# Kernel optimization log

Hardware: AMD Instinct MI355X
Metric: run time of the kernel (lower is better)

Reference implementation:

```python
import jax, jax.numpy as jnp
import numpy as np

B, N, F_IN, T = 4, 10000, 16, 12
E = 160000
K = 3
C_CHEB = 64
C_TIME = 64
LN_EPS = 1e-5


def _lambda_max(row, col, n):
    # Power iteration on the unnormalized Laplacian L = D - A (what
    # LaplacianLambdaMax computes with normalization=None).
    deg = np.bincount(row, minlength=n).astype(np.float64)
    rng = np.random.default_rng(123)
    v = rng.standard_normal(n)
    v /= np.linalg.norm(v)
    for _ in range(100):
        agg = np.zeros(n)
        np.add.at(agg, col, v[row])
        w = deg * v - agg
        v = w / max(np.linalg.norm(w), 1e-12)
    agg = np.zeros(n)
    np.add.at(agg, col, v[row])
    return np.float32(v @ (deg * v - agg))


def setup_inputs() -> dict:
    rng = np.random.default_rng(0)
    ei = rng.integers(0, N, size=(2, E))
    lam = _lambda_max(ei[0], ei[1], N)
    key = jax.random.key(0)
    k = jax.random.split(key, 8)
    sF = 1.0 / np.sqrt(F_IN)
    sC = 1.0 / np.sqrt(3 * C_CHEB)
    return {
        "x": jax.random.normal(k[0], (B, N, F_IN, T), jnp.float32),
        "edge_index": jnp.asarray(ei, dtype=jnp.int32),
        "lambda_max": jnp.float32(lam),
        "cheb_W": jax.random.normal(k[1], (K, F_IN, C_CHEB), jnp.float32) * sF,
        "cheb_b": jax.random.normal(k[2], (C_CHEB,), jnp.float32) * 0.01,
        "time_W": jax.random.normal(k[3], (C_TIME, C_CHEB, 1, 3), jnp.float32) * sC,
        "time_b": jax.random.normal(k[4], (C_TIME,), jnp.float32) * 0.01,
        "res_W": jax.random.normal(k[5], (C_TIME, F_IN, 1, 1), jnp.float32) * sF,
        "res_b": jax.random.normal(k[6], (C_TIME,), jnp.float32) * 0.01,
        "ln_gamma": jnp.ones((C_TIME,), jnp.float32),
        "ln_beta": jnp.zeros((C_TIME,), jnp.float32),
    }


def reference(x, edge_index, lambda_max, cheb_W, cheb_b, time_W, time_b,
              res_W, res_b, ln_gamma, ln_beta):
    Bb, Nn, Fin, Tt = x.shape
    row, col = edge_index[0], edge_index[1]
    # deg from scatter of unit edge weights at row (PyG get_laplacian)
    deg = jax.ops.segment_sum(jnp.ones(row.shape[0], x.dtype), row, num_segments=Nn)

    # --- ChebConv over all (batch, time) slices jointly ---
    # (B,N,F,T) -> (N, B*T, F): node axis leading for gather/scatter
    v = jnp.transpose(x, (1, 0, 3, 2)).reshape(Nn, Bb * Tt, Fin)

    def Lhat(u):  # scaled Laplacian L_hat = 2(D - A)/lambda_max - I
        agg = jax.ops.segment_sum(u[row], col, num_segments=Nn)
        return (2.0 / lambda_max) * (deg[:, None, None] * u - agg) - u

    Tx0 = v
    out = jnp.einsum('nbf,fc->nbc', Tx0, cheb_W[0])
    Tx1 = Lhat(Tx0)
    out = out + jnp.einsum('nbf,fc->nbc', Tx1, cheb_W[1])
    for k in range(2, cheb_W.shape[0]):
        Tx2 = 2.0 * Lhat(Tx1) - Tx0
        out = out + jnp.einsum('nbf,fc->nbc', Tx2, cheb_W[k])
        Tx0, Tx1 = Tx1, Tx2
    spatial = jax.nn.relu(out + cheb_b)  # (N, B*T, C_cheb)

    # (N, B*T, C) -> (B, C, N, T) for NCHW temporal conv
    spatial = spatial.reshape(Nn, Bb, Tt, C_CHEB)
    spatial = jnp.transpose(spatial, (1, 3, 0, 2))  # (B,C,N,T)

    dn = ('NCHW', 'OIHW', 'NCHW')
    tc = jax.lax.conv_general_dilated(spatial, time_W, (1, 1), ((0, 0), (1, 1)),
                                      dimension_numbers=dn) + time_b[None, :, None, None]
    xr = jnp.transpose(x, (0, 2, 1, 3))  # (B,F,N,T)
    res = jax.lax.conv_general_dilated(xr, res_W, (1, 1), ((0, 0), (0, 0)),
                                       dimension_numbers=dn) + res_b[None, :, None, None]

    h = jax.nn.relu(res + tc)                  # (B, C_time, N, T)
    h = jnp.transpose(h, (0, 3, 2, 1))         # (B, T, N, C_time)
    mu = jnp.mean(h, axis=-1, keepdims=True)
    var = jnp.mean((h - mu) ** 2, axis=-1, keepdims=True)
    hn = (h - mu) * jax.lax.rsqrt(var + LN_EPS) * ln_gamma + ln_beta
    return jnp.transpose(hn, (0, 2, 3, 1))     # (B, N, C_time, T)
```

## Files before the change

### kernel.cpp

```cpp
#include <hip/hip_runtime.h>

typedef short bf16x8 __attribute__((ext_vector_type(8)));
typedef float f32x4 __attribute__((ext_vector_type(4)));

#define NN 10000
#define EE 160000
#define BB 4
#define TTT 12
#define FFF 16
#define CCC 64
#define BT 48
#define NF 768
#define SLOTS 64

#define TCS 72
#define SPS 72
#define HMS 68

#define WS_DEG     0u
#define WS_CNT     40960u
#define WS_CWT     81920u
#define WS_RWTB    90112u
#define WS_WKT     94208u
#define WS_CSRP    118784u
#define WS_VBF     2678784u
#define WS_TX1BF   18040320u

__device__ __forceinline__ unsigned short f2bf(float x){
    unsigned int u = __float_as_uint(x);
    u += 0x7FFFu + ((u >> 16) & 1u);
    return (unsigned short)(u >> 16);
}
__device__ __forceinline__ float bf2f(unsigned short h){
    return __uint_as_float(((unsigned int)h) << 16);
}

#define GMIN4(E)                                                                  \
    E.x = E.x < NN ? E.x : NN; E.y = E.y < NN ? E.y : NN;                         \
    E.z = E.z < NN ? E.z : NN; E.w = E.w < NN ? E.w : NN;

#define GATHER8(SRC, EA, EB, ACC0, ACC1, ACC2, ACC3, Q)                           \
    {                                                                             \
        ushort4 p0 = *(const ushort4*)&SRC[(size_t)EA.x * NF + (Q) * 4];          \
        ushort4 p1 = *(const ushort4*)&SRC[(size_t)EA.y * NF + (Q) * 4];          \
        ushort4 p2 = *(const ushort4*)&SRC[(size_t)EA.z * NF + (Q) * 4];          \
        ushort4 p3 = *(const ushort4*)&SRC[(size_t)EA.w * NF + (Q) * 4];          \
        ushort4 p4 = *(const ushort4*)&SRC[(size_t)EB.x * NF + (Q) * 4];          \
        ushort4 p5 = *(const ushort4*)&SRC[(size_t)EB.y * NF + (Q) * 4];          \
        ushort4 p6 = *(const ushort4*)&SRC[(size_t)EB.z * NF + (Q) * 4];          \
        ushort4 p7 = *(const ushort4*)&SRC[(size_t)EB.w * NF + (Q) * 4];          \
        ACC0 += bf2f(p0.x)+bf2f(p1.x)+bf2f(p2.x)+bf2f(p3.x)                       \
              + bf2f(p4.x)+bf2f(p5.x)+bf2f(p6.x)+bf2f(p7.x);                      \
        ACC1 += bf2f(p0.y)+bf2f(p1.y)+bf2f(p2.y)+bf2f(p3.y)                       \
              + bf2f(p4.y)+bf2f(p5.y)+bf2f(p6.y)+bf2f(p7.y);                      \
        ACC2 += bf2f(p0.z)+bf2f(p1.z)+bf2f(p2.z)+bf2f(p3.z)                       \
              + bf2f(p4.z)+bf2f(p5.z)+bf2f(p6.z)+bf2f(p7.z);                      \
        ACC3 += bf2f(p0.w)+bf2f(p1.w)+bf2f(p2.w)+bf2f(p3.w)                       \
              + bf2f(p4.w)+bf2f(p5.w)+bf2f(p6.w)+bf2f(p7.w);                      \
    }

__global__ __launch_bounds__(256) void k_setup(
    const float* __restrict__ x, const int* __restrict__ ei,
    const float* __restrict__ chW, const float* __restrict__ tW, const float* __restrict__ rW,
    float* __restrict__ deg, int* __restrict__ cnt, int* __restrict__ csrp,
    unsigned short* __restrict__ vbf, unsigned short* __restrict__ tx1bf,
    unsigned short* __restrict__ cWt, unsigned short* __restrict__ rWtb,
    unsigned short* __restrict__ wkt)
{
    int bid = blockIdx.x, tid = threadIdx.x;
    if (bid < 625){
        int e = bid * 256 + tid;
        if (e < EE) atomicAdd(&deg[ei[e]], 1.0f);
    } else if (bid < 1250){
        int e = (bid - 625) * 256 + tid;
        if (e < EE){
            int c = ei[EE + e];
            int slot = atomicAdd(&cnt[c], 1);
            if (slot < SLOTS) csrp[c * SLOTS + slot] = ei[e];
        }
    } else if (bid < 3125){
        int u = (bid - 1250) * 256 + tid;
        int n = u / 48, r = u - n * 48;
        int t = r >> 2, j = r & 3;
        #pragma unroll
        for (int b = 0; b < BB; ++b){
            const float* xp = x + (size_t)(b * NN + n) * 192;
            ushort4 w = { f2bf(xp[(4 * j + 0) * 12 + t]),
                          f2bf(xp[(4 * j + 1) * 12 + t]),
                          f2bf(xp[(4 * j + 2) * 12 + t]),
                          f2bf(xp[(4 * j + 3) * 12 + t]) };
            *(ushort4*)&vbf[(size_t)n * NF + b * 192 + t * 16 + j * 4] = w;
        }
    } else if (bid == 3125){
        if (tid < 192){
            ushort4 z = { 0, 0, 0, 0 };
            *(ushort4*)&vbf[(size_t)NN * NF + tid * 4]   = z;
            *(ushort4*)&tx1bf[(size_t)NN * NF + tid * 4] = z;
        }
    } else {
        int idx = (bid - 3126) * 256 + tid;
        if (idx < 4096){
            int c = idx >> 6, k = idx & 63;
            float v = 0.f;
            if (k < 48){ int kk = k >> 4, f = k & 15; v = chW[kk * 1024 + f * 64 + c]; }
            cWt[idx] = f2bf(v);
        } else if (idx < 6144){
            int j = idx - 4096;
            int o = j >> 5, k = j & 31;
            float v = (k < 16) ? rW[o * 16 + k] : 0.f;
            rWtb[j] = f2bf(v);
        } else {
            int j = idx - 6144;
            int kk = j >> 12; int r2 = j & 4095;
            int o = r2 >> 6, dc = r2 & 63;
            wkt[j] = f2bf(tW[(o * 64 + dc) * 3 + kk]);
        }
    }
}

__global__ __launch_bounds__(192) void k_lhat(
        const unsigned short* __restrict__ vbf, const float* __restrict__ deg,
        const int* __restrict__ cnt, const int* __restrict__ csrp,
        const float* __restrict__ lam, unsigned short* __restrict__ tx1bf){
    int n = blockIdx.x;
    int q = threadIdx.x;
    float s2 = 2.0f / lam[0];
    float dn = deg[n];
    int c = cnt[n]; c = c > SLOTS ? SLOTS : c;
    int iters = (c + 15) >> 4;
    const int4* cp = (const int4*)(csrp + n * SLOTS);
    float a0 = 0.f, a1 = 0.f, a2 = 0.f, a3 = 0.f;
    for (int it = 0; it < iters; ++it){
        int4 e0 = cp[it * 4], e1 = cp[it * 4 + 1];
        int4 e2 = cp[it * 4 + 2], e3 = cp[it * 4 + 3];
        GMIN4(e0) GMIN4(e1) GMIN4(e2) GMIN4(e3)
        GATHER8(vbf, e0, e1, a0, a1, a2, a3, q);
        GATHER8(vbf, e2, e3, a0, a1, a2, a3, q);
    }
    ushort4 hv = *(const ushort4*)&vbf[(size_t)n * NF + q * 4];
    float v0 = bf2f(hv.x), v1 = bf2f(hv.y), v2 = bf2f(hv.z), v3 = bf2f(hv.w);
    ushort4 o4 = { f2bf(s2 * (dn * v0 - a0) - v0),
                   f2bf(s2 * (dn * v1 - a1) - v1),
                   f2bf(s2 * (dn * v2 - a2) - v2),
                   f2bf(s2 * (dn * v3 - a3) - v3) };
    *(ushort4*)&tx1bf[(size_t)n * NF + q * 4] = o4;
}

__global__ __launch_bounds__(256) void k_fused(
    const unsigned short* __restrict__ vbf, const unsigned short* __restrict__ tx1bf,
    const float* __restrict__ deg, const int* __restrict__ cnt, const int* __restrict__ csrp,
    const float* __restrict__ lam,
    const unsigned short* __restrict__ cWt, const float* __restrict__ chebB,
    const unsigned short* __restrict__ wkt, const float* __restrict__ timeB,
    const unsigned short* __restrict__ rWtb, const float* __restrict__ resB,
    const float* __restrict__ gamma, const float* __restrict__ beta,
    float* __restrict__ out)
{
    __shared__ __align__(16) char smem[21120];
    unsigned short* spl  = (unsigned short*)smem;
    float2*         red  = (float2*)smem;
    unsigned short* tcat = (unsigned short*)(smem + 8064);
    float*          hmat = (float*)(smem + 8064);

    int n = blockIdx.x;
    int tid = threadIdx.x;

    {
        int rid = tid >> 5;
        int cc = tid & 31;
        int b = rid >> 1, p = (rid & 1) * 13;
        *(unsigned int*)&spl[(b * 14 + p) * SPS + cc * 2] = 0u;
    }

    if (tid < 192){
        float s2 = 2.0f / lam[0];
        float dn = deg[n];
        ushort4 hv = *(const ushort4*)&vbf[(size_t)n * NF + tid * 4];
        ushort4 hu = *(const ushort4*)&tx1bf[(size_t)n * NF + tid * 4];
        float a0 = 0.f, a1 = 0.f, a2 = 0.f, a3 = 0.f;
        int c = cnt[n]; c = c > SLOTS ? SLOTS : c;
        int iters = (c + 7) >> 3;
        const int4* cp = (const int4*)(csrp + n * SLOTS);
        for (int it = 0; it < iters; ++it){
            int4 e0 = cp[it * 2], e1 = cp[it * 2 + 1];
            GMIN4(e0) GMIN4(e1)
            GATHER8(tx1bf, e0, e1, a0, a1, a2, a3, tid);
        }
        float u0 = bf2f(hu.x), u1 = bf2f(hu.y), u2 = bf2f(hu.z), u3 = bf2f(hu.w);
        float v0 = bf2f(hv.x), v1 = bf2f(hv.y), v2 = bf2f(hv.z), v3 = bf2f(hv.w);
        ushort4 w2 = { f2bf(2.0f * (s2 * (dn * u0 - a0) - u0) - v0),
                       f2bf(2.0f * (s2 * (dn * u1 - a1) - u1) - v1),
                       f2bf(2.0f * (s2 * (dn * u2 - a2) - u2) - v2),
                       f2bf(2.0f * (s2 * (dn * u3 - a3) - u3) - v3) };
        ushort4 zz = { 0, 0, 0, 0 };
        int bt = tid >> 2, ch = tid & 3;
        *(ushort4*)&tcat[bt * TCS +      ch * 4] = hv;
        *(ushort4*)&tcat[bt * TCS + 16 + ch * 4] = hu;
        *(ushort4*)&tcat[bt * TCS + 32 + ch * 4] = w2;
        *(ushort4*)&tcat[bt * TCS + 48 + ch * 4] = zz;
    }
    __syncthreads();

    int lane = tid & 63;
    int nt   = tid >> 6;
    int ln   = lane & 15;
    int quad = lane >> 4;
    int q8   = quad * 8;
    int col  = nt * 16 + ln;

    {
        bf16x8 cb0 = *(const bf16x8*)&cWt[col * 64 + q8];
        bf16x8 cb1 = *(const bf16x8*)&cWt[col * 64 + 32 + q8];
        bf16x8 rb  = *(const bf16x8*)&rWtb[col * 32 + q8];
        f32x4 cacc[3], racc[3];
        #pragma unroll
        for (int mt = 0; mt < 3; ++mt){
            bf16x8 a0 = *(const bf16x8*)&tcat[(mt * 16 + ln) * TCS + q8];
            bf16x8 a1 = *(const bf16x8*)&tcat[(mt * 16 + ln) * TCS + 32 + q8];
            f32x4 z = {0.f, 0.f, 0.f, 0.f};
            cacc[mt] = __builtin_amdgcn_mfma_f32_16x16x32_bf16(a0, cb0, z, 0, 0, 0);
            cacc[mt] = __builtin_amdgcn_mfma_f32_16x16x32_bf16(a1, cb1, cacc[mt], 0, 0, 0);
            racc[mt] = __builtin_amdgcn_mfma_f32_16x16x32_bf16(a0, rb, z, 0, 0, 0);
        }
        float cb = chebB[col];
        #pragma unroll
        for (int mt = 0; mt < 3; ++mt){
            #pragma unroll
            for (int i = 0; i < 4; ++i){
                int r = mt * 16 + quad * 4 + i;
                int bb = (r * 43) >> 9;
                int tt = r - 12 * bb;
                float val = fmaxf(cacc[mt][i] + cb, 0.0f);
                spl[(bb * 14 + tt + 1) * SPS + col] = f2bf(val);
            }
        }
        __syncthreads();

        bf16x8 wb[3][2];
        #pragma unroll
        for (int kk = 0; kk < 3; ++kk){
            wb[kk][0] = *(const bf16x8*)&wkt[kk * 4096 + col * 64 + q8];
            wb[kk][1] = *(const bf16x8*)&wkt[kk * 4096 + col * 64 + 32 + q8];
        }
        float tb = timeB[col] + resB[col];
        #pragma unroll
        for (int mt = 0; mt < 3; ++mt){
            int bt = mt * 16 + ln;
            int bb = (bt * 43) >> 9;
            int tt = bt - 12 * bb;
            int rbase = bb * 14 + tt;
            f32x4 tacc = {0.f, 0.f, 0.f, 0.f};
            #pragma unroll
            for (int kk = 0; kk < 3; ++kk){
                bf16x8 a0 = *(const bf16x8*)&spl[(rbase + kk) * SPS + q8];
                bf16x8 a1 = *(const bf16x8*)&spl[(rbase + kk) * SPS + 32 + q8];
                tacc = __builtin_amdgcn_mfma_f32_16x16x32_bf16(a0, wb[kk][0], tacc, 0, 0, 0);
                tacc = __builtin_amdgcn_mfma_f32_16x16x32_bf16(a1, wb[kk][1], tacc, 0, 0, 0);
            }
            #pragma unroll
            for (int i = 0; i < 4; ++i){
                int r = mt * 16 + quad * 4 + i;
                float h = fmaxf(tacc[i] + racc[mt][i] + tb, 0.0f);
                hmat[r * HMS + col] = h;
            }
        }
    }
    __syncthreads();

    if (tid < 192){
        int row = tid >> 2, p = tid & 3;
        const float4* h4 = (const float4*)&hmat[row * HMS + p * 16];
        float4 A = h4[0], Bv = h4[1], Cv = h4[2], Dv = h4[3];
        float s = A.x+A.y+A.z+A.w + Bv.x+Bv.y+Bv.z+Bv.w
                + Cv.x+Cv.y+Cv.z+Cv.w + Dv.x+Dv.y+Dv.z+Dv.w;
        float q = A.x*A.x+A.y*A.y+A.z*A.z+A.w*A.w + Bv.x*Bv.x+Bv.y*Bv.y+Bv.z*Bv.z+Bv.w*Bv.w
                + Cv.x*Cv.x+Cv.y*Cv.y+Cv.z*Cv.z+Cv.w*Cv.w + Dv.x*Dv.x+Dv.y*Dv.y+Dv.z*Dv.z+Dv.w*Dv.w;
        s += __shfl_xor(s, 1); q += __shfl_xor(q, 1);
        s += __shfl_xor(s, 2); q += __shfl_xor(q, 2);
        if (p == 0) red[row] = make_float2(s, q);
    }
    __syncthreads();

    {
        int g = nt, o = lane;
        float gam = gamma[o], bet = beta[o];
        float res[12];
        #pragma unroll
        for (int t = 0; t < 12; ++t){
            int row = g * 12 + t;
            float h = hmat[row * HMS + o];
            float2 m = red[row];
            float mu  = m.x * (1.0f / 64.0f);
            float var = m.y * (1.0f / 64.0f) - mu * mu;
            float r   = rsqrtf(var + 1e-5f);
            res[t] = (h - mu) * r * gam + bet;
        }
        size_t obase = ((size_t)(g * NN + n) * CCC + o) * TTT;
        float4* op = (float4*)(out + obase);
        op[0] = make_float4(res[0], res[1], res[2],  res[3]);
        op[1] = make_float4(res[4], res[5], res[6],  res[7]);
        op[2] = make_float4(res[8], res[9], res[10], res[11]);
    }
}

extern "C" void kernel_launch(void* const* d_in, const int* in_sizes, int n_in,
                              void* d_out, int out_size, void* d_ws, size_t ws_size,
                              hipStream_t stream)
{
    (void)in_sizes; (void)n_in; (void)out_size; (void)ws_size;
    const float* x   = (const float*)d_in[0];
    const int*   ei  = (const int*)  d_in[1];
    const float* lam = (const float*)d_in[2];
    const float* chW = (const float*)d_in[3];
    const float* chB = (const float*)d_in[4];
    const float* tW  = (const float*)d_in[5];
    const float* tB  = (const float*)d_in[6];
    const float* rW  = (const float*)d_in[7];
    const float* rB  = (const float*)d_in[8];
    const float* gam = (const float*)d_in[9];
    const float* bet = (const float*)d_in[10];
    float* out = (float*)d_out;

    char* ws = (char*)d_ws;
    float* deg  = (float*)(ws + WS_DEG);
    int*   cnt  = (int*)  (ws + WS_CNT);
    unsigned short* cWt  = (unsigned short*)(ws + WS_CWT);
    unsigned short* rWtb = (unsigned short*)(ws + WS_RWTB);
    unsigned short* wkt  = (unsigned short*)(ws + WS_WKT);
    int*   csrp = (int*)  (ws + WS_CSRP);
    unsigned short* vbf   = (unsigned short*)(ws + WS_VBF);
    unsigned short* tx1bf = (unsigned short*)(ws + WS_TX1BF);

    hipMemsetAsync(ws, 0, 81920, stream);
    hipMemsetAsync(ws + WS_CSRP, 0x7F, NN * SLOTS * 4, stream);
    k_setup  <<<3198, 256, 0, stream>>>(x, ei, chW, tW, rW, deg, cnt, csrp,
                                        vbf, tx1bf, cWt, rWtb, wkt);
    k_lhat   <<<NN, 192, 0, stream>>>(vbf, deg, cnt, csrp, lam, tx1bf);
    k_fused  <<<NN, 256, 0, stream>>>(vbf, tx1bf, deg, cnt, csrp, lam,
                                      cWt, chB, wkt, tB, rWtb, rB, gam, bet, out);
}
```

Before: 281.3 us.

## Pack bf16 gather accumulation, vectorize input transpose, hoist weight loads, pad LDS

Several micro-optimizations at once. The neighbor gather now loads 8-byte words and accumulates into packed float2 vectors so the compiler can use packed FP32 adds, and the fused kernel's second-hop gather is unrolled to 16 edges per iteration. The input transpose in setup handles two timesteps per thread with float2 loads, which cuts the setup grid. Weight and bias loads in the fused kernel are hoisted before the gather so their latency overlaps it, and the spatial LDS row stride is padded from 72 to 80 to change bank mapping, at the cost of more shared memory and register pressure.

```diff
diff --git a/kernel.cpp b/kernel.cpp
--- a/kernel.cpp
+++ b/kernel.cpp
@@ -2,6 +2,7 @@
 
 typedef short bf16x8 __attribute__((ext_vector_type(8)));
 typedef float f32x4 __attribute__((ext_vector_type(4)));
+typedef float f32x2 __attribute__((ext_vector_type(2)));
 
 #define NN 10000
 #define EE 160000
@@ -14,7 +15,7 @@
 #define SLOTS 64
 
 #define TCS 72
-#define SPS 72
+#define SPS 80
 #define HMS 68
 
 #define WS_DEG     0u
@@ -39,24 +40,30 @@
     E.x = E.x < NN ? E.x : NN; E.y = E.y < NN ? E.y : NN;                         \
     E.z = E.z < NN ? E.z : NN; E.w = E.w < NN ? E.w : NN;
 
-#define GATHER8(SRC, EA, EB, ACC0, ACC1, ACC2, ACC3, Q)                           \
+#define ACCPK(D, AXY, AZW)                                                        \
     {                                                                             \
-        ushort4 p0 = *(const ushort4*)&SRC[(size_t)EA.x * NF + (Q) * 4];          \
-        ushort4 p1 = *(const ushort4*)&SRC[(size_t)EA.y * NF + (Q) * 4];          \
-        ushort4 p2 = *(const ushort4*)&SRC[(size_t)EA.z * NF + (Q) * 4];          \
-        ushort4 p3 = *(const ushort4*)&SRC[(size_t)EA.w * NF + (Q) * 4];          \
-        ushort4 p4 = *(const ushort4*)&SRC[(size_t)EB.x * NF + (Q) * 4];          \
-        ushort4 p5 = *(const ushort4*)&SRC[(size_t)EB.y * NF + (Q) * 4];          \
-        ushort4 p6 = *(const ushort4*)&SRC[(size_t)EB.z * NF + (Q) * 4];          \
-        ushort4 p7 = *(const ushort4*)&SRC[(size_t)EB.w * NF + (Q) * 4];          \
-        ACC0 += bf2f(p0.x)+bf2f(p1.x)+bf2f(p2.x)+bf2f(p3.x)                       \
-              + bf2f(p4.x)+bf2f(p5.x)+bf2f(p6.x)+bf2f(p7.x);                      \
-        ACC1 += bf2f(p0.y)+bf2f(p1.y)+bf2f(p2.y)+bf2f(p3.y)                       \
-              + bf2f(p4.y)+bf2f(p5.y)+bf2f(p6.y)+bf2f(p7.y);                      \
-        ACC2 += bf2f(p0.z)+bf2f(p1.z)+bf2f(p2.z)+bf2f(p3.z)                       \
-              + bf2f(p4.z)+bf2f(p5.z)+bf2f(p6.z)+bf2f(p7.z);                      \
-        ACC3 += bf2f(p0.w)+bf2f(p1.w)+bf2f(p2.w)+bf2f(p3.w)                       \
-              + bf2f(p4.w)+bf2f(p5.w)+bf2f(p6.w)+bf2f(p7.w);                      \
+        f32x2 t0, t1;                                                             \
+        t0.x = __uint_as_float((D).x << 16);                                      \
+        t0.y = __uint_as_float((D).x & 0xFFFF0000u);                              \
+        t1.x = __uint_as_float((D).y << 16);                                      \
+        t1.y = __uint_as_float((D).y & 0xFFFF0000u);                              \
+        AXY += t0; AZW += t1;                                                     \
+    }
+
+#define GATHER8PK(SRC, EA, EB, AXY, AZW, Q)                                       \
+    {                                                                             \
+        uint2 d0 = *(const uint2*)&SRC[(size_t)EA.x * NF + (Q) * 4];              \
+        uint2 d1 = *(const uint2*)&SRC[(size_t)EA.y * NF + (Q) * 4];              \
+        uint2 d2 = *(const uint2*)&SRC[(size_t)EA.z * NF + (Q) * 4];              \
+        uint2 d3 = *(const uint2*)&SRC[(size_t)EA.w * NF + (Q) * 4];              \
+        uint2 d4 = *(const uint2*)&SRC[(size_t)EB.x * NF + (Q) * 4];              \
+        uint2 d5 = *(const uint2*)&SRC[(size_t)EB.y * NF + (Q) * 4];              \
+        uint2 d6 = *(const uint2*)&SRC[(size_t)EB.z * NF + (Q) * 4];              \
+        uint2 d7 = *(const uint2*)&SRC[(size_t)EB.w * NF + (Q) * 4];              \
+        ACCPK(d0, AXY, AZW) ACCPK(d1, AXY, AZW)                                   \
+        ACCPK(d2, AXY, AZW) ACCPK(d3, AXY, AZW)                                   \
+        ACCPK(d4, AXY, AZW) ACCPK(d5, AXY, AZW)                                   \
+        ACCPK(d6, AXY, AZW) ACCPK(d7, AXY, AZW)                                   \
     }
 
 __global__ __launch_bounds__(256) void k_setup(
@@ -78,27 +85,33 @@
             int slot = atomicAdd(&cnt[c], 1);
             if (slot < SLOTS) csrp[c * SLOTS + slot] = ei[e];
         }
-    } else if (bid < 3125){
+    } else if (bid < 2188){
         int u = (bid - 1250) * 256 + tid;
-        int n = u / 48, r = u - n * 48;
-        int t = r >> 2, j = r & 3;
-        #pragma unroll
-        for (int b = 0; b < BB; ++b){
-            const float* xp = x + (size_t)(b * NN + n) * 192;
-            ushort4 w = { f2bf(xp[(4 * j + 0) * 12 + t]),
-                          f2bf(xp[(4 * j + 1) * 12 + t]),
-                          f2bf(xp[(4 * j + 2) * 12 + t]),
-                          f2bf(xp[(4 * j + 3) * 12 + t]) };
-            *(ushort4*)&vbf[(size_t)n * NF + b * 192 + t * 16 + j * 4] = w;
-        }
-    } else if (bid == 3125){
+        if (u < 240000){
+            int n = u / 24, r = u - n * 24;
+            int t2 = r >> 2, j = r & 3;
+            #pragma unroll
+            for (int b = 0; b < BB; ++b){
+                const float* xp = x + (size_t)(b * NN + n) * 192;
+                float2 v0 = *(const float2*)&xp[(4 * j + 0) * 12 + 2 * t2];
+                float2 v1 = *(const float2*)&xp[(4 * j + 1) * 12 + 2 * t2];
+                float2 v2 = *(const float2*)&xp[(4 * j + 2) * 12 + 2 * t2];
+                float2 v3 = *(const float2*)&xp[(4 * j + 3) * 12 + 2 * t2];
+                ushort4 w0 = { f2bf(v0.x), f2bf(v1.x), f2bf(v2.x), f2bf(v3.x) };
+                ushort4 w1 = { f2bf(v0.y), f2bf(v1.y), f2bf(v2.y), f2bf(v3.y) };
+                size_t base = (size_t)n * NF + b * 192 + (2 * t2) * 16 + j * 4;
+                *(ushort4*)&vbf[base]      = w0;
+                *(ushort4*)&vbf[base + 16] = w1;
+            }
+        }
+    } else if (bid == 2188){
         if (tid < 192){
             ushort4 z = { 0, 0, 0, 0 };
             *(ushort4*)&vbf[(size_t)NN * NF + tid * 4]   = z;
             *(ushort4*)&tx1bf[(size_t)NN * NF + tid * 4] = z;
         }
     } else {
-        int idx = (bid - 3126) * 256 + tid;
+        int idx = (bid - 2189) * 256 + tid;
         if (idx < 4096){
             int c = idx >> 6, k = idx & 63;
             float v = 0.f;
@@ -129,14 +142,15 @@
     int c = cnt[n]; c = c > SLOTS ? SLOTS : c;
     int iters = (c + 15) >> 4;
     const int4* cp = (const int4*)(csrp + n * SLOTS);
-    float a0 = 0.f, a1 = 0.f, a2 = 0.f, a3 = 0.f;
+    f32x2 Axy = {0.f, 0.f}, Azw = {0.f, 0.f};
     for (int it = 0; it < iters; ++it){
         int4 e0 = cp[it * 4], e1 = cp[it * 4 + 1];
         int4 e2 = cp[it * 4 + 2], e3 = cp[it * 4 + 3];
         GMIN4(e0) GMIN4(e1) GMIN4(e2) GMIN4(e3)
-        GATHER8(vbf, e0, e1, a0, a1, a2, a3, q);
-        GATHER8(vbf, e2, e3, a0, a1, a2, a3, q);
-    }
+        GATHER8PK(vbf, e0, e1, Axy, Azw, q);
+        GATHER8PK(vbf, e2, e3, Axy, Azw, q);
+    }
+    float a0 = Axy.x, a1 = Axy.y, a2 = Azw.x, a3 = Azw.y;
     ushort4 hv = *(const ushort4*)&vbf[(size_t)n * NF + q * 4];
     float v0 = bf2f(hv.x), v1 = bf2f(hv.y), v2 = bf2f(hv.z), v3 = bf2f(hv.w);
     ushort4 o4 = { f2bf(s2 * (dn * v0 - a0) - v0),
@@ -156,14 +170,27 @@
     const float* __restrict__ gamma, const float* __restrict__ beta,
     float* __restrict__ out)
 {
-    __shared__ __align__(16) char smem[21120];
+    __shared__ __align__(16) char smem[22016];
     unsigned short* spl  = (unsigned short*)smem;
     float2*         red  = (float2*)smem;
-    unsigned short* tcat = (unsigned short*)(smem + 8064);
-    float*          hmat = (float*)(smem + 8064);
+    unsigned short* tcat = (unsigned short*)(smem + 8960);
+    float*          hmat = (float*)(smem + 8960);
 
     int n = blockIdx.x;
     int tid = threadIdx.x;
+
+    int lane = tid & 63;
+    int nt   = tid >> 6;
+    int ln   = lane & 15;
+    int quad = lane >> 4;
+    int q8   = quad * 8;
+    int col  = nt * 16 + ln;
+
+    bf16x8 cb0 = *(const bf16x8*)&cWt[col * 64 + q8];
+    bf16x8 cb1 = *(const bf16x8*)&cWt[col * 64 + 32 + q8];
+    bf16x8 rb  = *(const bf16x8*)&rWtb[col * 32 + q8];
+    float cb = chebB[col];
+    float tb = timeB[col] + resB[col];
 
     {
         int rid = tid >> 5;
@@ -177,15 +204,18 @@
         float dn = deg[n];
         ushort4 hv = *(const ushort4*)&vbf[(size_t)n * NF + tid * 4];
         ushort4 hu = *(const ushort4*)&tx1bf[(size_t)n * NF + tid * 4];
-        float a0 = 0.f, a1 = 0.f, a2 = 0.f, a3 = 0.f;
+        f32x2 Axy = {0.f, 0.f}, Azw = {0.f, 0.f};
         int c = cnt[n]; c = c > SLOTS ? SLOTS : c;
-        int iters = (c + 7) >> 3;
+        int iters = (c + 15) >> 4;
         const int4* cp = (const int4*)(csrp + n * SLOTS);
         for (int it = 0; it < iters; ++it){
-            int4 e0 = cp[it * 2], e1 = cp[it * 2 + 1];
-            GMIN4(e0) GMIN4(e1)
-            GATHER8(tx1bf, e0, e1, a0, a1, a2, a3, tid);
-        }
+            int4 e0 = cp[it * 4], e1 = cp[it * 4 + 1];
+            int4 e2 = cp[it * 4 + 2], e3 = cp[it * 4 + 3];
+            GMIN4(e0) GMIN4(e1) GMIN4(e2) GMIN4(e3)
+            GATHER8PK(tx1bf, e0, e1, Axy, Azw, tid);
+            GATHER8PK(tx1bf, e2, e3, Axy, Azw, tid);
+        }
+        float a0 = Axy.x, a1 = Axy.y, a2 = Azw.x, a3 = Azw.y;
         float u0 = bf2f(hu.x), u1 = bf2f(hu.y), u2 = bf2f(hu.z), u3 = bf2f(hu.w);
         float v0 = bf2f(hv.x), v1 = bf2f(hv.y), v2 = bf2f(hv.z), v3 = bf2f(hv.w);
         ushort4 w2 = { f2bf(2.0f * (s2 * (dn * u0 - a0) - u0) - v0),
@@ -201,17 +231,7 @@
     }
     __syncthreads();
 
-    int lane = tid & 63;
-    int nt   = tid >> 6;
-    int ln   = lane & 15;
-    int quad = lane >> 4;
-    int q8   = quad * 8;
-    int col  = nt * 16 + ln;
-
     {
-        bf16x8 cb0 = *(const bf16x8*)&cWt[col * 64 + q8];
-        bf16x8 cb1 = *(const bf16x8*)&cWt[col * 64 + 32 + q8];
-        bf16x8 rb  = *(const bf16x8*)&rWtb[col * 32 + q8];
         f32x4 cacc[3], racc[3];
         #pragma unroll
         for (int mt = 0; mt < 3; ++mt){
@@ -222,7 +242,6 @@
             cacc[mt] = __builtin_amdgcn_mfma_f32_16x16x32_bf16(a1, cb1, cacc[mt], 0, 0, 0);
             racc[mt] = __builtin_amdgcn_mfma_f32_16x16x32_bf16(a0, rb, z, 0, 0, 0);
         }
-        float cb = chebB[col];
         #pragma unroll
         for (int mt = 0; mt < 3; ++mt){
             #pragma unroll
@@ -242,7 +261,6 @@
             wb[kk][0] = *(const bf16x8*)&wkt[kk * 4096 + col * 64 + q8];
             wb[kk][1] = *(const bf16x8*)&wkt[kk * 4096 + col * 64 + 32 + q8];
         }
-        float tb = timeB[col] + resB[col];
         #pragma unroll
         for (int mt = 0; mt < 3; ++mt){
             int bt = mt * 16 + ln;
@@ -333,7 +351,7 @@
 
     hipMemsetAsync(ws, 0, 81920, stream);
     hipMemsetAsync(ws + WS_CSRP, 0x7F, NN * SLOTS * 4, stream);
-    k_setup  <<<3198, 256, 0, stream>>>(x, ei, chW, tW, rW, deg, cnt, csrp,
+    k_setup  <<<2261, 256, 0, stream>>>(x, ei, chW, tW, rW, deg, cnt, csrp,
                                         vbf, tx1bf, cWt, rWtb, wkt);
     k_lhat   <<<NN, 192, 0, stream>>>(vbf, deg, cnt, csrp, lam, tx1bf);
     k_fused  <<<NN, 256, 0, stream>>>(vbf, tx1bf, deg, cnt, csrp, lam,
```

New measurement: 288.2 us. 2.4% more time.
